# Kernel optimization log

Hardware: AMD Instinct MI355X
Metric: run time of the kernel (lower is better)

The kernel has to match this reference:

```python
import jax, jax.numpy as jnp
import numpy as np

WS = 7   # w_size
K = 9    # k_neighbors


def setup_inputs() -> dict:
    key = jax.random.key(0)
    ks = jax.random.split(key, 6)
    B, C, H, W = 16, 64, 112, 112
    Cf = C // 4
    return {
        'x_in': jax.random.normal(ks[0], (B, C, H, W), jnp.float32),
        'Wf': jax.random.normal(ks[1], (Cf, C), jnp.float32) / np.sqrt(C).astype(np.float32),
        'bf': jnp.zeros((Cf,), jnp.float32),
        'Wp': jax.random.normal(ks[2], (C, Cf), jnp.float32) / np.sqrt(Cf).astype(np.float32),
        'bp': jnp.zeros((C,), jnp.float32),
        'W1': jax.random.normal(ks[3], (4, 2), jnp.float32) / np.sqrt(2.0).astype(np.float32),
        'b1': jnp.zeros((4,), jnp.float32),
        'W2': jax.random.normal(ks[4], (1, 4), jnp.float32) / 2.0,
        'b2': jnp.zeros((1,), jnp.float32),
        'sigma': jnp.asarray(4.0, jnp.float32),
        'alpha': jnp.asarray(0.5, jnp.float32),
    }


def reference(x_in, Wf, bf, Wp, bp, W1, b1, W2, b2, sigma, alpha):
    B, C, H, W = x_in.shape
    w, h = H // WS, W // WS                      # per-window spatial dims
    Bp, N = B * WS * WS, w * h                   # num windows, nodes per window
    # window partition: b c (Wg w) (Hg h) -> (b Wg Hg) c w h
    x = x_in.reshape(B, C, WS, w, WS, h).transpose(0, 2, 4, 1, 3, 5).reshape(Bp, C, w, h)
    # 1x1 conv f: dim -> dim//4
    f = jnp.einsum('bchw,oc->bohw', x, Wf) + bf[None, :, None, None]
    Cf = f.shape[1]
    xf = f.reshape(Bp, Cf, N).transpose(0, 2, 1)          # [Bp, N, Cf] node features
    # all-pairs cosine similarity (torch eps=1e-8)
    xn = xf / jnp.maximum(jnp.linalg.norm(xf, axis=-1, keepdims=True), 1e-8)
    sim_feat = jnp.einsum('bnc,bmc->bnm', xn, xn)         # [Bp, N, N]
    # spatial gaussian similarity
    ii, jj = jnp.meshgrid(jnp.arange(w), jnp.arange(h), indexing='ij')
    coords = jnp.stack([ii, jj], -1).reshape(N, 2).astype(jnp.float32)
    dist = jnp.sqrt(jnp.sum((coords[:, None] - coords[None]) ** 2, -1))
    sim_dist = jnp.exp(-dist ** 2 / (2.0 * sigma ** 2))   # [N, N]
    combined = alpha * sim_feat + (1.0 - alpha) * sim_dist[None]
    _, idx = jax.lax.top_k(combined, K)                   # [Bp, N, K] neighbor ids
    # gather neighbor messages; edges of node n are exactly its K top-k columns
    msg = xf[jnp.arange(Bp)[:, None, None], idx]          # [Bp, N, K, Cf]
    sf = jnp.take_along_axis(sim_feat, idx, axis=-1)      # edge cosine sim
    sd = sim_dist[jnp.arange(N)[:, None], idx]            # edge spatial sim
    pair = jnp.stack([sf, sd], -1)                        # [Bp, N, K, 2]
    hdn = jax.nn.silu(pair @ W1.T + b1)
    wgt = jax.nn.sigmoid(hdn @ W2.T + b2)[..., 0]         # [Bp, N, K]
    # scatter_add over edge_index[0] == per-source sum over its K edges
    wn = wgt / (jnp.sum(wgt, -1, keepdims=True) + 1e-12)
    out = jnp.einsum('bnk,bnkc->bnc', wn, msg)            # [Bp, N, Cf]
    out = out.reshape(Bp, w, h, Cf).transpose(0, 3, 1, 2)
    # window un-partition: (b Wg Hg) c w h -> b c (Wg w) (Hg h)
    out = out.reshape(B, WS, WS, Cf, w, h).transpose(0, 3, 1, 4, 2, 5).reshape(B, Cf, H, W)
    # 1x1 conv p: dim//4 -> dim, then flatten(2)
    y = jnp.einsum('bchw,oc->bohw', out, Wp) + bp[None, :, None, None]
    return y.reshape(B, C, H * W)
```

## Files before the change

### kernel.cpp

```cpp
#include <hip/hip_runtime.h>
#include <math.h>

#define CC    64
#define CF    16
#define NPIX  256
#define KK    9
#define HWQ   12544
#define WWQ   112
#define NTILE 784
#define NROWS (NTILE * NPIX)

__global__ __launch_bounds__(64, 4) void feat_k(
    const float* __restrict__ x_in, const float* __restrict__ Wf,
    const float* __restrict__ bf,
    float* __restrict__ xn_g, float* __restrict__ nrm_g)
{
    __shared__ float s_Wt[CC * CF];
    __shared__ float s_bf[CF];
    const int tid = threadIdx.x;
    for (int idx = tid; idx < CC * CF; idx += 64) {
        int c = idx >> 4, o = idx & 15;
        s_Wt[idx] = Wf[o * CC + c];
    }
    if (tid < CF) s_bf[tid] = bf[tid];
    __syncthreads();

    const int p    = blockIdx.x * 64 + tid;
    const int tile = p >> 8, pix = p & 255;
    const int bb = tile / 49, ssb = tile % 49;
    const int s1 = ssb / 7, s2 = ssb % 7;
    const int gy = s1 * 16 + (pix >> 4), gx = s2 * 16 + (pix & 15);
    const float* xb = x_in + (size_t)bb * CC * HWQ + (size_t)gy * WWQ + gx;

    float fv[CF];
    #pragma unroll
    for (int o = 0; o < CF; ++o) fv[o] = 0.0f;
    #pragma unroll 8
    for (int c = 0; c < CC; ++c) {
        float xv = xb[(size_t)c * HWQ];
        const float4* w4 = reinterpret_cast<const float4*>(&s_Wt[c << 4]);
        float4 w0 = w4[0], w1 = w4[1], w2 = w4[2], w3 = w4[3];
        fv[0]  = fmaf(xv, w0.x, fv[0]);  fv[1]  = fmaf(xv, w0.y, fv[1]);
        fv[2]  = fmaf(xv, w0.z, fv[2]);  fv[3]  = fmaf(xv, w0.w, fv[3]);
        fv[4]  = fmaf(xv, w1.x, fv[4]);  fv[5]  = fmaf(xv, w1.y, fv[5]);
        fv[6]  = fmaf(xv, w1.z, fv[6]);  fv[7]  = fmaf(xv, w1.w, fv[7]);
        fv[8]  = fmaf(xv, w2.x, fv[8]);  fv[9]  = fmaf(xv, w2.y, fv[9]);
        fv[10] = fmaf(xv, w2.z, fv[10]); fv[11] = fmaf(xv, w2.w, fv[11]);
        fv[12] = fmaf(xv, w3.x, fv[12]); fv[13] = fmaf(xv, w3.y, fv[13]);
        fv[14] = fmaf(xv, w3.z, fv[14]); fv[15] = fmaf(xv, w3.w, fv[15]);
    }
    #pragma unroll
    for (int o = 0; o < CF; ++o) fv[o] += s_bf[o];

    float ss2 = 0.0f;
    #pragma unroll
    for (int o = 0; o < CF; ++o) ss2 = fmaf(fv[o], fv[o], ss2);
    float nrm = fmaxf(sqrtf(ss2), 1e-8f);

    float xn[CF];
    #pragma unroll
    for (int o = 0; o < CF; ++o) xn[o] = fv[o] / nrm;

    float4* dst = reinterpret_cast<float4*>(xn_g + (size_t)p * CF);
    dst[0] = make_float4(xn[0],  xn[1],  xn[2],  xn[3]);
    dst[1] = make_float4(xn[4],  xn[5],  xn[6],  xn[7]);
    dst[2] = make_float4(xn[8],  xn[9],  xn[10], xn[11]);
    dst[3] = make_float4(xn[12], xn[13], xn[14], xn[15]);
    nrm_g[p] = nrm;
}

#define DOT16(dot, X, a0, a1, a2, a3)                                \
    dot = fmaf(X[0],  (a0).x, dot); dot = fmaf(X[1],  (a0).y, dot);  \
    dot = fmaf(X[2],  (a0).z, dot); dot = fmaf(X[3],  (a0).w, dot);  \
    dot = fmaf(X[4],  (a1).x, dot); dot = fmaf(X[5],  (a1).y, dot);  \
    dot = fmaf(X[6],  (a1).z, dot); dot = fmaf(X[7],  (a1).w, dot);  \
    dot = fmaf(X[8],  (a2).x, dot); dot = fmaf(X[9],  (a2).y, dot);  \
    dot = fmaf(X[10], (a2).z, dot); dot = fmaf(X[11], (a2).w, dot);  \
    dot = fmaf(X[12], (a3).x, dot); dot = fmaf(X[13], (a3).y, dot);  \
    dot = fmaf(X[14], (a3).z, dot); dot = fmaf(X[15], (a3).w, dot);

#define TOP9_INS(S, cv, ci) {                                        \
    const bool g0 = (cv) > tv0##S; const bool g1 = (cv) > tv1##S;    \
    const bool g2 = (cv) > tv2##S; const bool g3 = (cv) > tv3##S;    \
    const bool g4 = (cv) > tv4##S; const bool g5 = (cv) > tv5##S;    \
    const bool g6 = (cv) > tv6##S; const bool g7 = (cv) > tv7##S;    \
    const bool g8 = (cv) > tv8##S;                                   \
    const float nv0 = g0 ? (cv) : tv0##S;                            \
    const float nv1 = __builtin_amdgcn_fmed3f((cv), tv0##S, tv1##S); \
    const float nv2 = __builtin_amdgcn_fmed3f((cv), tv1##S, tv2##S); \
    const float nv3 = __builtin_amdgcn_fmed3f((cv), tv2##S, tv3##S); \
    const float nv4 = __builtin_amdgcn_fmed3f((cv), tv3##S, tv4##S); \
    const float nv5 = __builtin_amdgcn_fmed3f((cv), tv4##S, tv5##S); \
    const float nv6 = __builtin_amdgcn_fmed3f((cv), tv5##S, tv6##S); \
    const float nv7 = __builtin_amdgcn_fmed3f((cv), tv6##S, tv7##S); \
    const float nv8 = __builtin_amdgcn_fmed3f((cv), tv7##S, tv8##S); \
    const int nt0 = g0 ? (ci) : ti0##S;                              \
    const int nt1 = g0 ? ti0##S : (g1 ? (ci) : ti1##S);              \
    const int nt2 = g1 ? ti1##S : (g2 ? (ci) : ti2##S);              \
    const int nt3 = g2 ? ti2##S : (g3 ? (ci) : ti3##S);              \
    const int nt4 = g3 ? ti3##S : (g4 ? (ci) : ti4##S);              \
    const int nt5 = g4 ? ti4##S : (g5 ? (ci) : ti5##S);              \
    const int nt6 = g5 ? ti5##S : (g6 ? (ci) : ti6##S);              \
    const int nt7 = g6 ? ti6##S : (g7 ? (ci) : ti7##S);              \
    const int nt8 = g7 ? ti7##S : (g8 ? (ci) : ti8##S);              \
    tv0##S = nv0; tv1##S = nv1; tv2##S = nv2; tv3##S = nv3;          \
    tv4##S = nv4; tv5##S = nv5; tv6##S = nv6; tv7##S = nv7;          \
    tv8##S = nv8;                                                    \
    ti0##S = nt0; ti1##S = nt1; ti2##S = nt2; ti3##S = nt3;          \
    ti4##S = nt4; ti5##S = nt5; ti6##S = nt6; ti7##S = nt7;          \
    ti8##S = nt8; }

#define SIM_ITER2(MJ) {                                              \
    const int m = mbase + (MJ);                                      \
    const float4* xm4 =                                              \
        reinterpret_cast<const float4*>(&s_xn[m][0]);                \
    const float4 a0 = xm4[0], a1 = xm4[1], a2 = xm4[2], a3 = xm4[3]; \
    float dotA = 0.0f, dotB = 0.0f;                                  \
    DOT16(dotA, xnrA, a0, a1, a2, a3);                               \
    DOT16(dotB, xnrB, a0, a1, a2, a3);                               \
    const int dj = pj - (MJ);                                        \
    const int dj2 = dj * dj;                                         \
    const float sA = s_tabA[d2iA + dj2];                             \
    const float sB = s_tabA[d2iB + dj2];                             \
    const float combA = __fadd_rn(__fmul_rn(alpha, dotA), sA);       \
    const float combB = __fadd_rn(__fmul_rn(alpha, dotB), sB);       \
    TOP9_INS(A, combA, m)                                            \
    TOP9_INS(B, combB, m) }

#define SIM_ROW16_2()                                                \
        SIM_ITER2(0)  SIM_ITER2(1)  SIM_ITER2(2)  SIM_ITER2(3)       \
        SIM_ITER2(4)  SIM_ITER2(5)  SIM_ITER2(6)  SIM_ITER2(7)       \
        SIM_ITER2(8)  SIM_ITER2(9)  SIM_ITER2(10) SIM_ITER2(11)      \
        SIM_ITER2(12) SIM_ITER2(13) SIM_ITER2(14) SIM_ITER2(15)

#define EPILOGUE(TV, TI, PI, PJ) {                                   \
    float wk[KK]; float wsum = 0.0f;                                 \
    _Pragma("unroll")                                                \
    for (int k = 0; k < KK; ++k) {                                   \
        int m = TI[k];                                               \
        int di = (PI) - (m >> 4);                                    \
        int dj = (PJ) - (m & 15);                                    \
        float sd = s_tab[di * di + dj * dj];                         \
        float sf = (TV[k] - __fmul_rn(oma, sd)) / alpha;             \
        float hsum = b2r;                                            \
        _Pragma("unroll")                                            \
        for (int h = 0; h < 4; ++h) {                                \
            float z  = fmaf(sf, W1r[2*h], fmaf(sd, W1r[2*h+1], b1r[h])); \
            float sg = 1.0f / (1.0f + expf(-z));                     \
            hsum = fmaf(z * sg, W2r[h], hsum);                       \
        }                                                            \
        float wg = 1.0f / (1.0f + expf(-hsum));                      \
        wk[k] = wg; wsum += wg;                                      \
    }                                                                \
    wsum += 1e-12f;                                                  \
    float outv[CF];                                                  \
    _Pragma("unroll")                                                \
    for (int o = 0; o < CF; ++o) outv[o] = 0.0f;                     \
    _Pragma("unroll")                                                \
    for (int k = 0; k < KK; ++k) {                                   \
        const int m = TI[k];                                         \
        const float wnm = (wk[k] / wsum) * s_nrm[m];                 \
        const float4* xf4 = reinterpret_cast<const float4*>(&s_xn[m][0]); \
        float4 m0 = xf4[0], m1 = xf4[1], m2 = xf4[2], m3 = xf4[3];   \
        outv[0]  = fmaf(wnm, m0.x, outv[0]);  outv[1]  = fmaf(wnm, m0.y, outv[1]);  \
        outv[2]  = fmaf(wnm, m0.z, outv[2]);  outv[3]  = fmaf(wnm, m0.w, outv[3]);  \
        outv[4]  = fmaf(wnm, m1.x, outv[4]);  outv[5]  = fmaf(wnm, m1.y, outv[5]);  \
        outv[6]  = fmaf(wnm, m1.z, outv[6]);  outv[7]  = fmaf(wnm, m1.w, outv[7]);  \
        outv[8]  = fmaf(wnm, m2.x, outv[8]);  outv[9]  = fmaf(wnm, m2.y, outv[9]);  \
        outv[10] = fmaf(wnm, m2.z, outv[10]); outv[11] = fmaf(wnm, m2.w, outv[11]); \
        outv[12] = fmaf(wnm, m3.x, outv[12]); outv[13] = fmaf(wnm, m3.y, outv[13]); \
        outv[14] = fmaf(wnm, m3.z, outv[14]); outv[15] = fmaf(wnm, m3.w, outv[15]); \
    }                                                                \
    const int gy = s1 * 16 + (PI), gx = s2 * 16 + (PJ);              \
    float* yb = y + (size_t)bb * CC * HWQ + (size_t)gy * WWQ + gx;   \
    _Pragma("unroll 4")                                              \
    for (int o = 0; o < CC; ++o) {                                   \
        const float4* w4 = reinterpret_cast<const float4*>(&Wp[o * CF]); \
        float4 w0 = w4[0], w1 = w4[1], w2 = w4[2], w3 = w4[3];       \
        float acc = 0.0f;                                            \
        acc = fmaf(outv[0],  w0.x, acc); acc = fmaf(outv[1],  w0.y, acc); \
        acc = fmaf(outv[2],  w0.z, acc); acc = fmaf(outv[3],  w0.w, acc); \
        acc = fmaf(outv[4],  w1.x, acc); acc = fmaf(outv[5],  w1.y, acc); \
        acc = fmaf(outv[6],  w1.z, acc); acc = fmaf(outv[7],  w1.w, acc); \
        acc = fmaf(outv[8],  w2.x, acc); acc = fmaf(outv[9],  w2.y, acc); \
        acc = fmaf(outv[10], w2.z, acc); acc = fmaf(outv[11], w2.w, acc); \
        acc = fmaf(outv[12], w3.x, acc); acc = fmaf(outv[13], w3.y, acc); \
        acc = fmaf(outv[14], w3.z, acc); acc = fmaf(outv[15], w3.w, acc); \
        yb[(size_t)o * HWQ] = acc + bp[o];                           \
    } }

__global__ __launch_bounds__(128, 2) void gnn_2row(
    const float* __restrict__ xn_g, const float* __restrict__ nrm_g,
    const float* __restrict__ Wp,   const float* __restrict__ bp,
    const float* __restrict__ W1,   const float* __restrict__ b1,
    const float* __restrict__ W2,   const float* __restrict__ b2,
    const float* __restrict__ sigma_p, const float* __restrict__ alpha_p,
    float* __restrict__ y)
{
    __shared__ float s_xn[NPIX][CF];
    __shared__ float s_nrm[NPIX];
    __shared__ float s_tab[451];
    __shared__ float s_tabA[451];

    const int tile = blockIdx.x;
    const int bb = tile / 49, ssb = tile % 49;
    const int s1 = ssb / 7, s2 = ssb % 7;
    const int tid = threadIdx.x;

    const float alpha = alpha_p[0];
    const float oma   = 1.0f - alpha;
    const float sig   = sigma_p[0];
    const float denom = 2.0f * sig * sig;

    for (int t = tid; t < 451; t += 128) {
        float dd = sqrtf((float)t);
        float v  = expf((-(dd * dd)) / denom);
        s_tab[t]  = v;
        s_tabA[t] = __fmul_rn(oma, v);
    }
    const float* xt = xn_g + (size_t)tile * NPIX * CF;
    {
        const float4* src = reinterpret_cast<const float4*>(xt);
        float4*       dst = reinterpret_cast<float4*>(&s_xn[0][0]);
        #pragma unroll
        for (int i = 0; i < 8; ++i) dst[tid + i * 128] = src[tid + i * 128];
        const float* nsrc = nrm_g + (size_t)tile * NPIX;
        s_nrm[tid]       = nsrc[tid];
        s_nrm[tid + 128] = nsrc[tid + 128];
    }
    float W1r[8], b1r[4], W2r[4];
    #pragma unroll
    for (int h = 0; h < 8; ++h) W1r[h] = W1[h];
    #pragma unroll
    for (int h = 0; h < 4; ++h) { b1r[h] = b1[h]; W2r[h] = W2[h]; }
    const float b2r = b2[0];
    __syncthreads();

    const int rA  = tid;
    const int rB  = tid + 128;
    const int piA = rA >> 4;
    const int piB = piA + 8;
    const int pj  = rA & 15;

    float xnrA[CF], xnrB[CF];
    {
        const float4* xa = reinterpret_cast<const float4*>(&s_xn[rA][0]);
        float4 a0 = xa[0], a1 = xa[1], a2 = xa[2], a3 = xa[3];
        xnrA[0]=a0.x;  xnrA[1]=a0.y;  xnrA[2]=a0.z;  xnrA[3]=a0.w;
        xnrA[4]=a1.x;  xnrA[5]=a1.y;  xnrA[6]=a1.z;  xnrA[7]=a1.w;
        xnrA[8]=a2.x;  xnrA[9]=a2.y;  xnrA[10]=a2.z; xnrA[11]=a2.w;
        xnrA[12]=a3.x; xnrA[13]=a3.y; xnrA[14]=a3.z; xnrA[15]=a3.w;
        const float4* xb4 = reinterpret_cast<const float4*>(&s_xn[rB][0]);
        float4 b0 = xb4[0], b1v = xb4[1], b2v = xb4[2], b3 = xb4[3];
        xnrB[0]=b0.x;  xnrB[1]=b0.y;  xnrB[2]=b0.z;  xnrB[3]=b0.w;
        xnrB[4]=b1v.x; xnrB[5]=b1v.y; xnrB[6]=b1v.z; xnrB[7]=b1v.w;
        xnrB[8]=b2v.x; xnrB[9]=b2v.y; xnrB[10]=b2v.z; xnrB[11]=b2v.w;
        xnrB[12]=b3.x; xnrB[13]=b3.y; xnrB[14]=b3.z; xnrB[15]=b3.w;
    }

    float tv0A,tv1A,tv2A,tv3A,tv4A,tv5A,tv6A,tv7A,tv8A;
    int   ti0A,ti1A,ti2A,ti3A,ti4A,ti5A,ti6A,ti7A,ti8A;
    float tv0B,tv1B,tv2B,tv3B,tv4B,tv5B,tv6B,tv7B,tv8B;
    int   ti0B,ti1B,ti2B,ti3B,ti4B,ti5B,ti6B,ti7B,ti8B;
    tv0A=tv1A=tv2A=tv3A=tv4A=tv5A=tv6A=tv7A=tv8A = -INFINITY;
    ti0A=ti1A=ti2A=ti3A=ti4A=ti5A=ti6A=ti7A=ti8A = 0;
    tv0B=tv1B=tv2B=tv3B=tv4B=tv5B=tv6B=tv7B=tv8B = -INFINITY;
    ti0B=ti1B=ti2B=ti3B=ti4B=ti5B=ti6B=ti7B=ti8B = 0;

    #pragma unroll 1
    for (int mi = 0; mi < 16; ++mi) {
        const int diA   = piA - mi;
        const int diB   = piB - mi;
        const int d2iA  = diA * diA;
        const int d2iB  = diB * diB;
        const int mbase = mi << 4;
        SIM_ROW16_2()
    }

    const float tvA[KK] = {tv0A,tv1A,tv2A,tv3A,tv4A,tv5A,tv6A,tv7A,tv8A};
    const int   tiA[KK] = {ti0A,ti1A,ti2A,ti3A,ti4A,ti5A,ti6A,ti7A,ti8A};
    const float tvB[KK] = {tv0B,tv1B,tv2B,tv3B,tv4B,tv5B,tv6B,tv7B,tv8B};
    const int   tiB[KK] = {ti0B,ti1B,ti2B,ti3B,ti4B,ti5B,ti6B,ti7B,ti8B};

    EPILOGUE(tvA, tiA, piA, pj)
    EPILOGUE(tvB, tiB, piB, pj)
}

__global__ __launch_bounds__(256) void gnn_fused(
    const float* __restrict__ x_in, const float* __restrict__ Wf,
    const float* __restrict__ bf,   const float* __restrict__ Wp,
    const float* __restrict__ bp,   const float* __restrict__ W1,
    const float* __restrict__ b1,   const float* __restrict__ W2,
    const float* __restrict__ b2,   const float* __restrict__ sigma_p,
    const float* __restrict__ alpha_p, float* __restrict__ y)
{
    __shared__ float s_xf[NPIX][CF];
    __shared__ float s_xn[NPIX][CF];
    __shared__ float s_W[CC * CF];
    __shared__ float s_table[451];
    __shared__ float s_bias[CC];

    const int bpi = blockIdx.x;
    const int bb  = bpi / 49;
    const int ssb = bpi % 49;
    const int s1  = ssb / 7, s2 = ssb % 7;
    const int tid = threadIdx.x;
    const int pi  = tid >> 4, pj = tid & 15;
    const int gy  = s1 * 16 + pi, gx = s2 * 16 + pj;

    const float alpha = alpha_p[0];
    const float oma   = 1.0f - alpha;
    const float sig   = sigma_p[0];
    const float denom = 2.0f * sig * sig;

    for (int t = tid; t < CF * CC; t += NPIX) s_W[t] = Wf[t];
    if (tid < CF) s_bias[tid] = bf[tid];
    for (int t = tid; t < 451; t += NPIX) {
        float dd = sqrtf((float)t);
        s_table[t] = expf((-(dd * dd)) / denom);
    }
    float W1r[8], b1r[4], W2r[4];
    #pragma unroll
    for (int h = 0; h < 8; ++h) W1r[h] = W1[h];
    #pragma unroll
    for (int h = 0; h < 4; ++h) { b1r[h] = b1[h]; W2r[h] = W2[h]; }
    const float b2r = b2[0];
    __syncthreads();

    const float* xb = x_in + (size_t)bb * CC * HWQ + (size_t)gy * WWQ + gx;
    float fv[CF];
    #pragma unroll
    for (int o = 0; o < CF; ++o) fv[o] = 0.0f;
    for (int c = 0; c < CC; ++c) {
        float xv = xb[(size_t)c * HWQ];
        #pragma unroll
        for (int o = 0; o < CF; ++o)
            fv[o] = fmaf(xv, s_W[o * CC + c], fv[o]);
    }
    #pragma unroll
    for (int o = 0; o < CF; ++o) fv[o] += s_bias[o];

    float ss2 = 0.0f;
    #pragma unroll
    for (int o = 0; o < CF; ++o) ss2 = fmaf(fv[o], fv[o], ss2);
    float nrm = fmaxf(sqrtf(ss2), 1e-8f);

    float xnr[CF];
    #pragma unroll
    for (int o = 0; o < CF; ++o) {
        xnr[o] = fv[o] / nrm;
        s_xf[tid][o] = fv[o];
        s_xn[tid][o] = xnr[o];
    }
    __syncthreads();

    float tv[KK]; int ti[KK];
    #pragma unroll
    for (int k = 0; k < KK; ++k) { tv[k] = -INFINITY; ti[k] = 0; }

    for (int m = 0; m < NPIX; ++m) {
        const float4* xm4 = reinterpret_cast<const float4*>(&s_xn[m][0]);
        float4 a0 = xm4[0], a1 = xm4[1], a2 = xm4[2], a3 = xm4[3];
        float dot = 0.0f;
        dot = fmaf(xnr[0],  a0.x, dot); dot = fmaf(xnr[1],  a0.y, dot);
        dot = fmaf(xnr[2],  a0.z, dot); dot = fmaf(xnr[3],  a0.w, dot);
        dot = fmaf(xnr[4],  a1.x, dot); dot = fmaf(xnr[5],  a1.y, dot);
        dot = fmaf(xnr[6],  a1.z, dot); dot = fmaf(xnr[7],  a1.w, dot);
        dot = fmaf(xnr[8],  a2.x, dot); dot = fmaf(xnr[9],  a2.y, dot);
        dot = fmaf(xnr[10], a2.z, dot); dot = fmaf(xnr[11], a2.w, dot);
        dot = fmaf(xnr[12], a3.x, dot); dot = fmaf(xnr[13], a3.y, dot);
        dot = fmaf(xnr[14], a3.z, dot); dot = fmaf(xnr[15], a3.w, dot);

        int di = pi - (m >> 4);
        int dj = pj - (m & 15);
        float sd = s_table[di * di + dj * dj];
        float comb = __fadd_rn(__fmul_rn(alpha, dot), __fmul_rn(oma, sd));

        if (comb > tv[KK - 1]) {
            float cv = comb; int ci = m;
            #pragma unroll
            for (int t = KK - 1; t >= 0; --t) {
                bool g = (cv > tv[t]);
                float ov = tv[t]; int oi = ti[t];
                if (g) {
                    if (t + 1 < KK) { tv[t + 1] = ov; ti[t + 1] = oi; }
                    tv[t] = cv; ti[t] = ci;
                }
            }
        }
    }

    float wk[KK];
    float wsum = 0.0f;
    #pragma unroll
    for (int k = 0; k < KK; ++k) {
        int m = ti[k];
        int di = pi - (m >> 4);
        int dj = pj - (m & 15);
        float sd = s_table[di * di + dj * dj];
        float sf = (tv[k] - __fmul_rn(oma, sd)) / alpha;
        float hsum = b2r;
        #pragma unroll
        for (int h = 0; h < 4; ++h) {
            float z  = fmaf(sf, W1r[2 * h], fmaf(sd, W1r[2 * h + 1], b1r[h]));
            float sg = 1.0f / (1.0f + expf(-z));
            hsum = fmaf(z * sg, W2r[h], hsum);
        }
        float wg = 1.0f / (1.0f + expf(-hsum));
        wk[k] = wg;
        wsum += wg;
    }
    wsum += 1e-12f;

    float outv[CF];
    #pragma unroll
    for (int o = 0; o < CF; ++o) outv[o] = 0.0f;
    #pragma unroll
    for (int k = 0; k < KK; ++k) {
        float wn = wk[k] / wsum;
        int m = ti[k];
        const float4* xf4 = reinterpret_cast<const float4*>(&s_xf[m][0]);
        float4 m0 = xf4[0], m1 = xf4[1], m2 = xf4[2], m3 = xf4[3];
        outv[0]  = fmaf(wn, m0.x, outv[0]);  outv[1]  = fmaf(wn, m0.y, outv[1]);
        outv[2]  = fmaf(wn, m0.z, outv[2]);  outv[3]  = fmaf(wn, m0.w, outv[3]);
        outv[4]  = fmaf(wn, m1.x, outv[4]);  outv[5]  = fmaf(wn, m1.y, outv[5]);
        outv[6]  = fmaf(wn, m1.z, outv[6]);  outv[7]  = fmaf(wn, m1.w, outv[7]);
        outv[8]  = fmaf(wn, m2.x, outv[8]);  outv[9]  = fmaf(wn, m2.y, outv[9]);
        outv[10] = fmaf(wn, m2.z, outv[10]); outv[11] = fmaf(wn, m2.w, outv[11]);
        outv[12] = fmaf(wn, m3.x, outv[12]); outv[13] = fmaf(wn, m3.y, outv[13]);
        outv[14] = fmaf(wn, m3.z, outv[14]); outv[15] = fmaf(wn, m3.w, outv[15]);
    }

    __syncthreads();
    for (int t = tid; t < CC * CF; t += NPIX) s_W[t] = Wp[t];
    if (tid < CC) s_bias[tid] = bp[tid];
    __syncthreads();

    float* yb = y + (size_t)bb * CC * HWQ + (size_t)gy * WWQ + gx;
    for (int o = 0; o < CC; ++o) {
        float acc = 0.0f;
        #pragma unroll
        for (int c = 0; c < CF; ++c)
            acc = fmaf(outv[c], s_W[o * CF + c], acc);
        yb[(size_t)o * HWQ] = acc + s_bias[o];
    }
}

extern "C" void kernel_launch(void* const* d_in, const int* in_sizes, int n_in,
                              void* d_out, int out_size, void* d_ws, size_t ws_size,
                              hipStream_t stream) {
    const float* x_in  = (const float*)d_in[0];
    const float* Wf    = (const float*)d_in[1];
    const float* bf    = (const float*)d_in[2];
    const float* Wp    = (const float*)d_in[3];
    const float* bp    = (const float*)d_in[4];
    const float* W1    = (const float*)d_in[5];
    const float* b1    = (const float*)d_in[6];
    const float* W2    = (const float*)d_in[7];
    const float* b2    = (const float*)d_in[8];
    const float* sigma = (const float*)d_in[9];
    const float* alpha = (const float*)d_in[10];
    float* y = (float*)d_out;

    const size_t need = (size_t)(NROWS * (CF + 1)) * sizeof(float);
    if (ws_size >= need) {
        float* xn_g  = (float*)d_ws;
        float* nrm_g = xn_g + (size_t)NROWS * CF;
        feat_k<<<3136, 64, 0, stream>>>(x_in, Wf, bf, xn_g, nrm_g);
        gnn_2row<<<NTILE, 128, 0, stream>>>(xn_g, nrm_g, Wp, bp, W1, b1,
                                            W2, b2, sigma, alpha, y);
    } else {
        gnn_fused<<<NTILE, NPIX, 0, stream>>>(x_in, Wf, bf, Wp, bp, W1, b1, W2,
                                              b2, sigma, alpha, y);
    }
}
```

Measured before the change: 151.4 us.

## Split top-k candidate scan across two thread halves and merge via LDS

The gnn_2row kernel now launches 256 threads per tile instead of 128. Each half scans 8 of the 16 candidate rows and keeps partial top-9 lists for its two query rows. The second half writes its partial lists to shared memory, and the first half merges them before running the epilogue. This doubles the parallelism in the dominant similarity/top-k scan. The cost is an extra barrier and merge, plus half the threads sitting idle during the epilogue.

```diff
diff --git a/kernel.cpp b/kernel.cpp
--- a/kernel.cpp
+++ b/kernel.cpp
@@ -132,6 +132,37 @@
         SIM_ITER2(4)  SIM_ITER2(5)  SIM_ITER2(6)  SIM_ITER2(7)       \
         SIM_ITER2(8)  SIM_ITER2(9)  SIM_ITER2(10) SIM_ITER2(11)      \
         SIM_ITER2(12) SIM_ITER2(13) SIM_ITER2(14) SIM_ITER2(15)
+
+#define PUBLISH_AB() {                                               \
+    s_pv[0][0][rl]=tv0A; s_pi[0][0][rl]=(unsigned short)ti0A;        \
+    s_pv[0][1][rl]=tv1A; s_pi[0][1][rl]=(unsigned short)ti1A;        \
+    s_pv[0][2][rl]=tv2A; s_pi[0][2][rl]=(unsigned short)ti2A;        \
+    s_pv[0][3][rl]=tv3A; s_pi[0][3][rl]=(unsigned short)ti3A;        \
+    s_pv[0][4][rl]=tv4A; s_pi[0][4][rl]=(unsigned short)ti4A;        \
+    s_pv[0][5][rl]=tv5A; s_pi[0][5][rl]=(unsigned short)ti5A;        \
+    s_pv[0][6][rl]=tv6A; s_pi[0][6][rl]=(unsigned short)ti6A;        \
+    s_pv[0][7][rl]=tv7A; s_pi[0][7][rl]=(unsigned short)ti7A;        \
+    s_pv[0][8][rl]=tv8A; s_pi[0][8][rl]=(unsigned short)ti8A;        \
+    s_pv[1][0][rl]=tv0B; s_pi[1][0][rl]=(unsigned short)ti0B;        \
+    s_pv[1][1][rl]=tv1B; s_pi[1][1][rl]=(unsigned short)ti1B;        \
+    s_pv[1][2][rl]=tv2B; s_pi[1][2][rl]=(unsigned short)ti2B;        \
+    s_pv[1][3][rl]=tv3B; s_pi[1][3][rl]=(unsigned short)ti3B;        \
+    s_pv[1][4][rl]=tv4B; s_pi[1][4][rl]=(unsigned short)ti4B;        \
+    s_pv[1][5][rl]=tv5B; s_pi[1][5][rl]=(unsigned short)ti5B;        \
+    s_pv[1][6][rl]=tv6B; s_pi[1][6][rl]=(unsigned short)ti6B;        \
+    s_pv[1][7][rl]=tv7B; s_pi[1][7][rl]=(unsigned short)ti7B;        \
+    s_pv[1][8][rl]=tv8B; s_pi[1][8][rl]=(unsigned short)ti8B; }
+
+#define MERGE_AB() {                                                 \
+    _Pragma("unroll")                                                \
+    for (int k = 0; k < KK; ++k) {                                   \
+        const float bvA = s_pv[0][k][rl];                            \
+        const int   biA = (int)s_pi[0][k][rl];                       \
+        TOP9_INS(A, bvA, biA)                                        \
+        const float bvB = s_pv[1][k][rl];                            \
+        const int   biB = (int)s_pi[1][k][rl];                       \
+        TOP9_INS(B, bvB, biB)                                        \
+    } }
 
 #define EPILOGUE(TV, TI, PI, PJ) {                                   \
     float wk[KK]; float wsum = 0.0f;                                 \
@@ -189,7 +220,7 @@
         yb[(size_t)o * HWQ] = acc + bp[o];                           \
     } }
 
-__global__ __launch_bounds__(128, 2) void gnn_2row(
+__global__ __launch_bounds__(256, 2) void gnn_2row(
     const float* __restrict__ xn_g, const float* __restrict__ nrm_g,
     const float* __restrict__ Wp,   const float* __restrict__ bp,
     const float* __restrict__ W1,   const float* __restrict__ b1,
@@ -201,18 +232,22 @@
     __shared__ float s_nrm[NPIX];
     __shared__ float s_tab[451];
     __shared__ float s_tabA[451];
+    __shared__ float s_pv[2][KK][128];
+    __shared__ unsigned short s_pi[2][KK][128];
 
     const int tile = blockIdx.x;
     const int bb = tile / 49, ssb = tile % 49;
     const int s1 = ssb / 7, s2 = ssb % 7;
     const int tid = threadIdx.x;
+    const int rl  = tid & 127;
+    const int ch  = tid >> 7;
 
     const float alpha = alpha_p[0];
     const float oma   = 1.0f - alpha;
     const float sig   = sigma_p[0];
     const float denom = 2.0f * sig * sig;
 
-    for (int t = tid; t < 451; t += 128) {
+    for (int t = tid; t < 451; t += 256) {
         float dd = sqrtf((float)t);
         float v  = expf((-(dd * dd)) / denom);
         s_tab[t]  = v;
@@ -223,10 +258,8 @@
         const float4* src = reinterpret_cast<const float4*>(xt);
         float4*       dst = reinterpret_cast<float4*>(&s_xn[0][0]);
         #pragma unroll
-        for (int i = 0; i < 8; ++i) dst[tid + i * 128] = src[tid + i * 128];
-        const float* nsrc = nrm_g + (size_t)tile * NPIX;
-        s_nrm[tid]       = nsrc[tid];
-        s_nrm[tid + 128] = nsrc[tid + 128];
+        for (int i = 0; i < 4; ++i) dst[tid + i * 256] = src[tid + i * 256];
+        s_nrm[tid] = nrm_g[(size_t)tile * NPIX + tid];
     }
     float W1r[8], b1r[4], W2r[4];
     #pragma unroll
@@ -236,8 +269,8 @@
     const float b2r = b2[0];
     __syncthreads();
 
-    const int rA  = tid;
-    const int rB  = tid + 128;
+    const int rA  = rl;
+    const int rB  = rl + 128;
     const int piA = rA >> 4;
     const int piB = piA + 8;
     const int pj  = rA & 15;
@@ -267,8 +300,10 @@
     tv0B=tv1B=tv2B=tv3B=tv4B=tv5B=tv6B=tv7B=tv8B = -INFINITY;
     ti0B=ti1B=ti2B=ti3B=ti4B=ti5B=ti6B=ti7B=ti8B = 0;
 
+    const int mi0 = ch << 3;
     #pragma unroll 1
-    for (int mi = 0; mi < 16; ++mi) {
+    for (int q = 0; q < 8; ++q) {
+        const int mi    = mi0 + q;
         const int diA   = piA - mi;
         const int diB   = piB - mi;
         const int d2iA  = diA * diA;
@@ -276,6 +311,11 @@
         const int mbase = mi << 4;
         SIM_ROW16_2()
     }
+
+    if (ch == 1) PUBLISH_AB()
+    __syncthreads();
+    if (ch == 1) return;
+    MERGE_AB()
 
     const float tvA[KK] = {tv0A,tv1A,tv2A,tv3A,tv4A,tv5A,tv6A,tv7A,tv8A};
     const int   tiA[KK] = {ti0A,ti1A,ti2A,ti3A,ti4A,ti5A,ti6A,ti7A,ti8A};
@@ -467,7 +507,7 @@
         float* xn_g  = (float*)d_ws;
         float* nrm_g = xn_g + (size_t)NROWS * CF;
         feat_k<<<3136, 64, 0, stream>>>(x_in, Wf, bf, xn_g, nrm_g);
-        gnn_2row<<<NTILE, 128, 0, stream>>>(xn_g, nrm_g, Wp, bp, W1, b1,
+        gnn_2row<<<NTILE, 256, 0, stream>>>(xn_g, nrm_g, Wp, bp, W1, b1,
                                             W2, b2, sigma, alpha, y);
     } else {
         gnn_fused<<<NTILE, NPIX, 0, stream>>>(x_in, Wf, bf, Wp, bp, W1, b1, W2,
```

After: 179.4 us. 1.18x slower.
